# Kernel tuning notes

Measured on AMD Instinct MI355X. Metric: run time of the kernel, lower is better.

Reference implementation:

```python
import jax, jax.numpy as jnp
import numpy as np

B, N, K, D, H, FF, L, NH = 8, 50, 20, 3, 128, 2048, 3, 8
S = N * K
HD = H // NH


def setup_inputs() -> dict:
    key = jax.random.key(0)
    ks = jax.random.split(key, 16)
    visited = jax.random.uniform(ks[0], (B, S)) < 0.05
    # the single most-recent action per batch row (status flips 0 -> 1)
    action_idx = jax.random.randint(ks[1], (B,), 0, S)
    visited = visited.at[jnp.arange(B), action_idx].set(True)
    feats = jax.random.normal(ks[2], (B, S, D - 1)) * visited[:, :, None]
    state = jnp.concatenate([feats, visited[:, :, None].astype(jnp.float32)], axis=-1)
    prev_state = state.at[jnp.arange(B), action_idx, :].set(0.0)

    def w(k, shape, s=0.02):
        return jax.random.normal(k, shape, dtype=jnp.float32) * s

    return dict(
        prev_state=prev_state, state=state,
        W_pre=w(ks[3], (D, H)), b_pre=jnp.zeros(H),
        Wq=w(ks[4], (L, H, H)), bq=jnp.zeros((L, H)),
        Wk=w(ks[5], (L, H, H)), bk=jnp.zeros((L, H)),
        Wv=w(ks[6], (L, H, H)), bv=jnp.zeros((L, H)),
        Wo=w(ks[7], (L, H, H)), bo=jnp.zeros((L, H)),
        ln1_g=jnp.ones((L, H)), ln1_b=jnp.zeros((L, H)),
        Wff1=w(ks[8], (L, H, FF)), bff1=jnp.zeros((L, FF)),
        Wff2=w(ks[9], (L, FF, H)), bff2=jnp.zeros((L, H)),
        ln2_g=jnp.ones((L, H)), ln2_b=jnp.zeros((L, H)),
        W_comb=w(ks[10], (2 * H, H)), b_comb=jnp.zeros(H),
        W_dec=w(ks[11], (H, H)), b_dec=jnp.zeros(H),
        W_lin=w(ks[12], (S, S)), b_lin=jnp.zeros(S),
    )


def _layer_norm(x, g, b, eps=1e-5):
    m = jnp.mean(x, -1, keepdims=True)
    v = jnp.mean(jnp.square(x - m), -1, keepdims=True)
    return (x - m) * jax.lax.rsqrt(v + eps) * g + b


def _update_mask(state):
    # vectorized equivalent of the original Python-loop scatter mask
    status = state[:, :, -1] != 0                      # visited [B, S], S = K*N channel-major
    mask = status
    vis_kn = status.reshape(B, K, N)
    user_any = vis_kn.any(axis=1)                      # [B, N]: user visited on any channel
    mask = mask | jnp.broadcast_to(user_any[:, None, :], (B, K, N)).reshape(B, S)
    assigned = state.reshape(B, K, N, D).sum(-1) != 0  # [B, K, N]
    full = assigned.sum(-1) >= 2                       # [B, K]: channel already has 2 users
    mask = mask | jnp.broadcast_to(full[:, :, None], (B, K, N)).reshape(B, S)
    return mask


def reference(prev_state, state, W_pre, b_pre, Wq, bq, Wk, bk, Wv, bv, Wo, bo,
              ln1_g, ln1_b, Wff1, bff1, Wff2, bff2, ln2_g, ln2_b,
              W_comb, b_comb, W_dec, b_dec, W_lin, b_lin):
    mask = _update_mask(state)
    # exactly one status change per batch row (sequential RL step)
    diff = prev_state[:, :, -1] != state[:, :, -1]
    act_idx = jnp.argmax(diff, axis=1)                 # [B]

    x = state @ W_pre + b_pre                          # [B, S, H]
    scale = np.float32(1.0 / np.sqrt(HD))
    for i in range(L):  # 3 post-LN transformer encoder layers
        q = (x @ Wq[i] + bq[i]).reshape(B, S, NH, HD)
        k = (x @ Wk[i] + bk[i]).reshape(B, S, NH, HD)
        v = (x @ Wv[i] + bv[i]).reshape(B, S, NH, HD)
        att = jax.nn.softmax(jnp.einsum('bqhd,bkhd->bhqk', q, k) * scale, axis=-1)
        o = jnp.einsum('bhqk,bkhd->bqhd', att, v).reshape(B, S, H) @ Wo[i] + bo[i]
        x = _layer_norm(x + o, ln1_g[i], ln1_b[i])
        ff = jax.nn.relu(x @ Wff1[i] + bff1[i]) @ Wff2[i] + bff2[i]
        x = _layer_norm(x + ff, ln2_g[i], ln2_b[i])

    last = x[jnp.arange(B), act_idx]                   # [B, H]
    combined = jnp.concatenate([x.mean(axis=1), last], axis=-1)  # [B, 2H]
    g = combined @ W_comb + b_comb                     # [B, H]
    dec = x @ W_dec + b_dec                            # [B, S, H]
    scores = jnp.einsum('bsh,bh->bs', dec, g)          # [B, S]
    masked = scores @ W_lin + b_lin                    # Q-Learning head
    return jnp.where(mask, -jnp.inf, masked)
```

## Files before the change

### kernel.cpp

```cpp
#include <hip/hip_runtime.h>
#include <math.h>

#define Bb 8
#define Ss 1000
#define Kk 20
#define Nn 50
#define Dd 3
#define Hh 128
#define FFf 2048
#define Ll 3
#define NHh 8
#define HDd 16
#define ROWS (Bb*Ss)

#define SENTINEL -3.0e38f

typedef unsigned short ush;
typedef short short8 __attribute__((ext_vector_type(8)));
typedef float f32x4 __attribute__((ext_vector_type(4)));

__device__ __forceinline__ ush f2b(float f) {
  unsigned x = __float_as_uint(f);
  return (ush)((x + 0x7fff + ((x >> 16) & 1)) >> 16);
}

__global__ __launch_bounds__(256) void mask_kernel(const float* __restrict__ state,
                                                   const float* __restrict__ prev_state,
                                                   int* __restrict__ mask, int* __restrict__ act_idx) {
  int b = blockIdx.x, tid = threadIdx.x;
  __shared__ unsigned char status[Ss], assigned[Ss], uany[Nn], fullk[Kk];
  __shared__ int act;
  if (tid == 0) act = 1 << 30;
  __syncthreads();
  for (int s = tid; s < Ss; s += 256) {
    const float* st = state + ((size_t)b * Ss + s) * Dd;
    float f2 = st[2];
    status[s] = (f2 != 0.f);
    assigned[s] = ((st[0] + st[1] + f2) != 0.f);
    float p2 = prev_state[((size_t)b * Ss + s) * Dd + 2];
    if (p2 != f2) atomicMin(&act, s);
  }
  __syncthreads();
  if (tid < Nn) {
    unsigned char a = 0;
    for (int k = 0; k < Kk; ++k) a |= status[k * Nn + tid];
    uany[tid] = a;
  } else if (tid >= 64 && tid < 64 + Kk) {
    int k = tid - 64, cnt = 0;
    for (int n = 0; n < Nn; ++n) cnt += assigned[k * Nn + n];
    fullk[k] = (cnt >= 2);
  }
  __syncthreads();
  for (int s = tid; s < Ss; s += 256)
    mask[b * Ss + s] = (int)(status[s] | uany[s % Nn] | fullk[s / Nn]);
  if (tid == 0) act_idx[b] = (act >= Ss) ? 0 : act;
}

__global__ __launch_bounds__(256) void pre_kernel(const float* __restrict__ state,
                                                  const float* __restrict__ W_pre,
                                                  const float* __restrict__ b_pre,
                                                  float* __restrict__ x, ush* __restrict__ xbf) {
  int idx = blockIdx.x * 256 + threadIdx.x;
  if (idx >= ROWS * Hh) return;
  int row = idx >> 7, n = idx & 127;
  const float* st = state + (size_t)row * Dd;
  float v = b_pre[n] + st[0] * W_pre[n] + st[1] * W_pre[Hh + n] + st[2] * W_pre[2 * Hh + n];
  x[idx] = v;
  xbf[idx] = f2b(v);
}

#define S1 (384*128)
#define S2 (128*128)
#define S3 (2048*128)
#define S4 (128*2048)
#define SPL (S1+S2+S3+S4)
__global__ __launch_bounds__(256) void wprep_kernel(const float* __restrict__ Wq, const float* __restrict__ Wk,
                                                    const float* __restrict__ Wv, const float* __restrict__ Wo,
                                                    const float* __restrict__ Wff1, const float* __restrict__ Wff2,
                                                    const float* __restrict__ bq, const float* __restrict__ bk,
                                                    const float* __restrict__ bv,
                                                    ush* __restrict__ wqkvT, ush* __restrict__ woT,
                                                    ush* __restrict__ wff1T, ush* __restrict__ wff2T,
                                                    float* __restrict__ bqkv) {
  int idx = blockIdx.x * 256 + threadIdx.x;
  if (idx < Ll * SPL) {
    int l = idx / SPL, r = idx % SPL;
    if (r < S1) {
      int k = r / 384, n = r % 384;
      float v = (n < 128) ? Wq[((size_t)l * Hh + k) * Hh + n]
              : (n < 256) ? Wk[((size_t)l * Hh + k) * Hh + (n - 128)]
                          : Wv[((size_t)l * Hh + k) * Hh + (n - 256)];
      wqkvT[((size_t)l * 384 + n) * 128 + k] = f2b(v);
    } else if (r < S1 + S2) {
      int rr = r - S1; int k = rr >> 7, n = rr & 127;
      woT[((size_t)l * 128 + n) * 128 + k] = f2b(Wo[((size_t)l * Hh + k) * Hh + n]);
    } else if (r < S1 + S2 + S3) {
      int rr = r - S1 - S2; int k = rr >> 11, n = rr & 2047;
      wff1T[((size_t)l * 2048 + n) * 128 + k] = f2b(Wff1[((size_t)l * Hh + k) * FFf + n]);
    } else {
      int rr = r - S1 - S2 - S3; int k = rr >> 7, n = rr & 127;
      wff2T[((size_t)l * 128 + n) * 2048 + k] = f2b(Wff2[((size_t)l * FFf + k) * Hh + n]);
    }
  }
  if (idx < Ll * 384) {
    int l = idx / 384, c = idx % 384;
    bqkv[idx] = (c < 128) ? bq[l * Hh + c] : (c < 256 ? bk[l * Hh + c - 128] : bv[l * Hh + c - 256]);
  }
}

#define LDP 40
template <int ABF16, int OBF16, int RELU, int PARTIAL, int QKVV>
__global__ __launch_bounds__(256) void gemm_mfma(const void* __restrict__ A, const ush* __restrict__ Wt,
                                                 const float* __restrict__ bias, void* __restrict__ out,
                                                 int M, int N, int K, int klen, ush* __restrict__ vTout) {
  __shared__ ush As[64 * LDP];
  __shared__ ush Bs[64 * LDP];
  int tid = threadIdx.x;
  int lane = tid & 63, wid = tid >> 6;
  int wr = wid >> 1, wc = wid & 1;
  int m0 = blockIdx.y * 64, n0 = blockIdx.x * 64;
  int lrow = tid >> 2, lk = (tid & 3) << 3;
  int quad = lane >> 4, l16 = lane & 15, kb = quad << 3;
  int kstart = PARTIAL ? blockIdx.z * klen : 0;

  f32x4 acc[2][2];
#pragma unroll
  for (int i = 0; i < 2; ++i)
#pragma unroll
    for (int j = 0; j < 2; ++j) acc[i][j] = (f32x4){0.f, 0.f, 0.f, 0.f};

  for (int k0 = kstart; k0 < kstart + klen; k0 += 32) {
    if (ABF16) {
      short8 av = *(const short8*)((const ush*)A + (size_t)(m0 + lrow) * K + k0 + lk);
      *(short8*)&As[lrow * LDP + lk] = av;
    } else {
      const float* ap = (const float*)A + (size_t)(m0 + lrow) * K + k0 + lk;
      short8 s;
#pragma unroll
      for (int i = 0; i < 8; ++i) s[i] = (short)f2b(ap[i]);
      *(short8*)&As[lrow * LDP + lk] = s;
    }
    short8 bv = *(const short8*)&Wt[(size_t)(n0 + lrow) * K + k0 + lk];
    *(short8*)&Bs[lrow * LDP + lk] = bv;
    __syncthreads();

    short8 a0 = *(short8*)&As[(wr * 32 + l16) * LDP + kb];
    short8 a1 = *(short8*)&As[(wr * 32 + 16 + l16) * LDP + kb];
    short8 b0 = *(short8*)&Bs[(wc * 32 + l16) * LDP + kb];
    short8 b1 = *(short8*)&Bs[(wc * 32 + 16 + l16) * LDP + kb];
    acc[0][0] = __builtin_amdgcn_mfma_f32_16x16x32_bf16(a0, b0, acc[0][0], 0, 0, 0);
    acc[0][1] = __builtin_amdgcn_mfma_f32_16x16x32_bf16(a0, b1, acc[0][1], 0, 0, 0);
    acc[1][0] = __builtin_amdgcn_mfma_f32_16x16x32_bf16(a1, b0, acc[1][0], 0, 0, 0);
    acc[1][1] = __builtin_amdgcn_mfma_f32_16x16x32_bf16(a1, b1, acc[1][1], 0, 0, 0);
    __syncthreads();
  }

  float* pout = PARTIAL ? ((float*)out + (size_t)blockIdx.z * M * N) : (float*)out;
#pragma unroll
  for (int i = 0; i < 2; ++i)
#pragma unroll
    for (int j = 0; j < 2; ++j) {
      int col = n0 + wc * 32 + j * 16 + l16;
      int rbase = m0 + wr * 32 + i * 16 + quad * 4;
      float bval = (!PARTIAL || blockIdx.z == 0) ? bias[col] : 0.f;
#pragma unroll
      for (int v = 0; v < 4; ++v) {
        float o = acc[i][j][v] + bval;
        if (RELU) o = fmaxf(o, 0.f);
        if (QKVV && col >= 256) {
          int row = rbase + v;
          int bb2 = row / 1000, qq = row - bb2 * 1000;
          vTout[((size_t)(bb2 * 128 + (col - 256))) * 1024 + qq] = f2b(o);
        } else if (OBF16) {
          ((ush*)out)[(size_t)(rbase + v) * N + col] = f2b(o);
        } else {
          pout[(size_t)(rbase + v) * N + col] = o;
        }
      }
    }
}

#define WLP 132
__global__ __launch_bounds__(256) void wo_ln_kernel(const ush* __restrict__ A, const ush* __restrict__ Wt,
                                                    const float* __restrict__ bias,
                                                    const float* __restrict__ ln_g, const float* __restrict__ ln_b,
                                                    float* __restrict__ x, ush* __restrict__ xbf) {
  __shared__ char smem[64 * WLP * 4];
  ush* As = (ush*)smem;
  ush* Bs = As + 64 * LDP;
  float* xs = (float*)smem;
  __shared__ float pbias[128], pg[128], pb2[128];

  int tid = threadIdx.x, lane = tid & 63, w = tid >> 6;
  int l16 = lane & 15, quad = lane >> 4, kb = quad * 8;
  int m0 = blockIdx.x * 64;
  if (tid < 128) { pbias[tid] = bias[tid]; pg[tid] = ln_g[tid]; pb2[tid] = ln_b[tid]; }

  f32x4 acc[8];
#pragma unroll
  for (int j = 0; j < 8; ++j) acc[j] = (f32x4){0.f, 0.f, 0.f, 0.f};

  int srow = tid >> 2, slk = (tid & 3) << 3;
  for (int k0 = 0; k0 < 128; k0 += 32) {
    *(short8*)&As[srow * LDP + slk] = *(const short8*)(A + (size_t)(m0 + srow) * 128 + k0 + slk);
#pragma unroll
    for (int rr = 0; rr < 2; ++rr) {
      int row = rr * 64 + srow;
      *(short8*)&Bs[row * LDP + slk] = *(const short8*)(Wt + (size_t)row * 128 + k0 + slk);
    }
    __syncthreads();
    short8 aA = *(short8*)&As[(w * 16 + l16) * LDP + kb];
#pragma unroll
    for (int j = 0; j < 8; ++j) {
      short8 bj = *(short8*)&Bs[(j * 16 + l16) * LDP + kb];
      acc[j] = __builtin_amdgcn_mfma_f32_16x16x32_bf16(aA, bj, acc[j], 0, 0, 0);
    }
    __syncthreads();
  }

  for (int e = tid; e < 64 * 32; e += 256) {
    int idx = e * 4; int row = idx >> 7, col = idx & 127;
    *(float4*)&xs[row * WLP + col] = *(const float4*)&x[(size_t)(m0 + row) * 128 + col];
  }
  __syncthreads();

  float v[8][4], s1[4] = {0.f, 0.f, 0.f, 0.f}, s2[4] = {0.f, 0.f, 0.f, 0.f};
#pragma unroll
  for (int j = 0; j < 8; ++j) {
    int col = j * 16 + l16;
#pragma unroll
    for (int r = 0; r < 4; ++r) {
      int rowt = w * 16 + quad * 4 + r;
      float vv = acc[j][r] + pbias[col] + xs[rowt * WLP + col];
      v[j][r] = vv; s1[r] += vv; s2[r] += vv * vv;
    }
  }
#pragma unroll
  for (int m = 1; m <= 8; m <<= 1) {
#pragma unroll
    for (int r = 0; r < 4; ++r) { s1[r] += __shfl_xor(s1[r], m); s2[r] += __shfl_xor(s2[r], m); }
  }
#pragma unroll
  for (int r = 0; r < 4; ++r) {
    int rowt = w * 16 + quad * 4 + r;
    float mean = s1[r] * (1.f / 128.f);
    float var = s2[r] * (1.f / 128.f) - mean * mean;
    float rstd = rsqrtf(var + 1e-5f);
#pragma unroll
    for (int j = 0; j < 8; ++j) {
      int col = j * 16 + l16;
      float o = (v[j][r] - mean) * rstd * pg[col] + pb2[col];
      size_t gi = (size_t)(m0 + rowt) * 128 + col;
      x[gi] = o; xbf[gi] = f2b(o);
    }
  }
}

__global__ __launch_bounds__(256) void attn_mfma(const ush* __restrict__ qkv,
                                                 const ush* __restrict__ vT,
                                                 ush* __restrict__ attn_o) {
  int blk = blockIdx.x;
  int local = blk >> 3;
  int bh = ((blk & 7) << 3) | (local >> 4);
  int qt = local & 15;
  int b = bh >> 3, h = bh & 7;
  int qbase = qt * 64;
  int tid = threadIdx.x, lane = tid & 63, w = tid >> 6;
  int l16 = lane & 15, quad = lane >> 4, kb = quad * 8;

  __shared__ ush Ks[64][40];
  __shared__ ush Vs[16][72];
  __shared__ ush Pb[4][16][72];

  if (tid < 128)
    *(short8*)&Ks[tid >> 1][16 + (tid & 1) * 8] = (short8){0, 0, 0, 0, 0, 0, 0, 0};

  int qrow = qbase + w * 16 + l16; if (qrow >= Ss) qrow = Ss - 1;
  short8 aq = *(const short8*)(qkv + (size_t)(b * Ss + qrow) * 384 + h * HDd + kb);

  const short one_b = (short)0x3F80;
  const short8 ones = (short8){one_b, one_b, one_b, one_b, one_b, one_b, one_b, one_b};
  f32x4 acc_pv = (f32x4){0.f, 0.f, 0.f, 0.f};
  f32x4 acc_l = (f32x4){0.f, 0.f, 0.f, 0.f};
  const f32x4 zero4 = (f32x4){0.f, 0.f, 0.f, 0.f};

  for (int k0 = 0; k0 < Ss; k0 += 64) {
    __syncthreads();
    if (tid < 128) {
      int row = tid >> 1, g = tid & 1;
      int key = k0 + row;
      short8 s8 = (short8){0, 0, 0, 0, 0, 0, 0, 0};
      if (key < Ss)
        s8 = *(const short8*)(qkv + (size_t)(b * Ss + key) * 384 + 128 + h * HDd + g * 8);
      *(short8*)&Ks[row][g * 8] = s8;
    } else {
      int t = tid - 128;
      int d = t >> 3, kg = t & 7;
      short8 v8 = *(const short8*)(vT + (size_t)(b * 128 + h * 16 + d) * 1024 + k0 + kg * 8);
      *(short8*)&Vs[d][kg * 8] = v8;
    }
    __syncthreads();

#pragma unroll
    for (int kn = 0; kn < 4; ++kn) {
      short8 bk = *(short8*)&Ks[kn * 16 + l16][kb];
      f32x4 s = __builtin_amdgcn_mfma_f32_16x16x32_bf16(aq, bk, zero4, 0, 0, 0);
      int key = k0 + kn * 16 + l16;
      float m = (key < Ss) ? 1.f : 0.f;
#pragma unroll
      for (int r = 0; r < 4; ++r)
        Pb[w][quad * 4 + r][kn * 16 + l16] = f2b(__expf(s[r] * 0.25f) * m);
    }
    short8 pa0 = *(short8*)&Pb[w][l16][kb];
    short8 pa1 = *(short8*)&Pb[w][l16][32 + kb];
    short8 vb0 = *(short8*)&Vs[l16][kb];
    short8 vb1 = *(short8*)&Vs[l16][32 + kb];
    acc_pv = __builtin_amdgcn_mfma_f32_16x16x32_bf16(pa0, vb0, acc_pv, 0, 0, 0);
    acc_pv = __builtin_amdgcn_mfma_f32_16x16x32_bf16(pa1, vb1, acc_pv, 0, 0, 0);
    acc_l = __builtin_amdgcn_mfma_f32_16x16x32_bf16(pa0, ones, acc_l, 0, 0, 0);
    acc_l = __builtin_amdgcn_mfma_f32_16x16x32_bf16(pa1, ones, acc_l, 0, 0, 0);
  }

#pragma unroll
  for (int r = 0; r < 4; ++r) {
    int q = qbase + w * 16 + quad * 4 + r;
    if (q < Ss)
      attn_o[((size_t)(b * Ss + q)) * Hh + h * HDd + l16] = f2b(acc_pv[r] / acc_l[r]);
  }
}

__global__ __launch_bounds__(256) void resid_ln_kernel(float* __restrict__ x, ush* __restrict__ xbf,
                                                       const float* __restrict__ r, int nparts, size_t pstride,
                                                       const float* __restrict__ g, const float* __restrict__ bb) {
  int half = threadIdx.x >> 7;
  int row = blockIdx.x * 2 + half;
  int n = threadIdx.x & 127;
  int wid = threadIdx.x >> 6;
  float v = x[(size_t)row * Hh + n];
  for (int p = 0; p < nparts; ++p) v += r[p * pstride + (size_t)row * Hh + n];
  float s = v;
  for (int off = 32; off; off >>= 1) s += __shfl_down(s, off);
  __shared__ float red[4], red2[4];
  if ((threadIdx.x & 63) == 0) red[wid] = s;
  __syncthreads();
  float mean = (red[half * 2] + red[half * 2 + 1]) * (1.f / Hh);
  float d = v - mean;
  float s2 = d * d;
  for (int off = 32; off; off >>= 1) s2 += __shfl_down(s2, off);
  if ((threadIdx.x & 63) == 0) red2[wid] = s2;
  __syncthreads();
  float var = (red2[half * 2] + red2[half * 2 + 1]) * (1.f / Hh);
  float o = d * rsqrtf(var + 1e-5f) * g[n] + bb[n];
  x[(size_t)row * Hh + n] = o;
  xbf[(size_t)row * Hh + n] = f2b(o);
}

__global__ __launch_bounds__(128) void mean_part_kernel(const float* __restrict__ x,
                                                        float* __restrict__ mpart) {
  int c = blockIdx.x, b = blockIdx.y, n = threadIdx.x;
  const float* xb = x + ((size_t)b * Ss + c * 125) * Hh + n;
  float s = 0.f;
#pragma unroll 5
  for (int i = 0; i < 125; ++i) s += xb[(size_t)i * Hh];
  mpart[(c * Bb + b) * Hh + n] = s;
}

__global__ __launch_bounds__(128) void ghc_kernel(const float* __restrict__ x, const float* __restrict__ mpart,
                                                  const int* __restrict__ act_idx,
                                                  const float* __restrict__ W_comb, const float* __restrict__ b_comb,
                                                  const float* __restrict__ W_dec, const float* __restrict__ b_dec,
                                                  float* __restrict__ h, float* __restrict__ cb) {
  int b = blockIdx.x, n = threadIdx.x;
  __shared__ float cs[2 * Hh], gs[Hh], red[2];
  float mean = 0.f;
#pragma unroll
  for (int c = 0; c < 8; ++c) mean += mpart[(c * Bb + b) * Hh + n];
  cs[n] = mean * (1.f / Ss);
  cs[Hh + n] = x[((size_t)b * Ss + act_idx[b]) * Hh + n];
  __syncthreads();
  float acc = b_comb[n];
  for (int j = 0; j < 2 * Hh; ++j) acc += cs[j] * W_comb[(size_t)j * Hh + n];
  gs[n] = acc;
  __syncthreads();
  float hv = 0.f;
  for (int c = 0; c < Hh; ++c) hv += W_dec[(size_t)n * Hh + c] * gs[c];
  h[b * Hh + n] = hv;
  float t = b_dec[n] * gs[n];
  for (int off = 32; off; off >>= 1) t += __shfl_down(t, off);
  if ((n & 63) == 0) red[n >> 6] = t;
  __syncthreads();
  if (n == 0) cb[b] = red[0] + red[1];
}

__global__ __launch_bounds__(256) void scores_kernel(const float* __restrict__ x, const float* __restrict__ h,
                                                     const float* __restrict__ cb, float* __restrict__ scores) {
  int wid = threadIdx.x >> 6, lane = threadIdx.x & 63;
  int row = blockIdx.x * 4 + wid;
  if (row >= ROWS) return;
  int b = row / Ss;
  const float* xr = x + (size_t)row * Hh;
  const float* hb = h + b * Hh;
  float s = xr[lane] * hb[lane] + xr[lane + 64] * hb[lane + 64];
  for (int off = 32; off; off >>= 1) s += __shfl_down(s, off);
  if (lane == 0) scores[row] = s + cb[b];
}

__global__ __launch_bounds__(256) void final_part(const float* __restrict__ scores,
                                                  const float* __restrict__ W_lin,
                                                  float* __restrict__ fpart) {
  int spc = blockIdx.x, kc = blockIdx.y, b = blockIdx.z;
  int tid = threadIdx.x;
  __shared__ float ss[125];
  for (int i = tid; i < 125; i += 256) ss[i] = scores[b * Ss + kc * 125 + i];
  __syncthreads();
  if (tid < 250) {
    int sp = spc * 250 + tid;
    float acc = 0.f;
    const float* wl = &W_lin[(size_t)(kc * 125) * Ss + sp];
#pragma unroll 5
    for (int s = 0; s < 125; ++s) acc = fmaf(ss[s], wl[(size_t)s * Ss], acc);
    fpart[((size_t)kc * Bb + b) * Ss + sp] = acc;
  }
}

__global__ __launch_bounds__(256) void final_combine(const float* __restrict__ fpart,
                                                     const float* __restrict__ b_lin,
                                                     const int* __restrict__ mask,
                                                     float* __restrict__ out) {
  int b = blockIdx.y;
  int sp = blockIdx.x * 256 + threadIdx.x;
  if (sp >= Ss) return;
  float acc = b_lin[sp];
#pragma unroll
  for (int kc = 0; kc < 8; ++kc) acc += fpart[((size_t)kc * Bb + b) * Ss + sp];
  out[b * Ss + sp] = mask[b * Ss + sp] ? SENTINEL : acc;
}

extern "C" void kernel_launch(void* const* d_in, const int* in_sizes, int n_in,
                              void* d_out, int out_size, void* d_ws, size_t ws_size,
                              hipStream_t stream) {
  const float* prev_state = (const float*)d_in[0];
  const float* state = (const float*)d_in[1];
  const float* W_pre = (const float*)d_in[2];
  const float* b_pre = (const float*)d_in[3];
  const float* Wq = (const float*)d_in[4];
  const float* bq = (const float*)d_in[5];
  const float* Wk = (const float*)d_in[6];
  const float* bk = (const float*)d_in[7];
  const float* Wv = (const float*)d_in[8];
  const float* bv = (const float*)d_in[9];
  const float* Wo = (const float*)d_in[10];
  const float* bo = (const float*)d_in[11];
  const float* ln1_g = (const float*)d_in[12];
  const float* ln1_b = (const float*)d_in[13];
  const float* Wff1 = (const float*)d_in[14];
  const float* bff1 = (const float*)d_in[15];
  const float* Wff2 = (const float*)d_in[16];
  const float* bff2 = (const float*)d_in[17];
  const float* ln2_g = (const float*)d_in[18];
  const float* ln2_b = (const float*)d_in[19];
  const float* W_comb = (const float*)d_in[20];
  const float* b_comb = (const float*)d_in[21];
  const float* W_dec = (const float*)d_in[22];
  const float* b_dec = (const float*)d_in[23];
  const float* W_lin = (const float*)d_in[24];
  const float* b_lin = (const float*)d_in[25];

  char* wsp = (char*)d_ws;
  auto alloc = [&](size_t bytes) { char* p = wsp; wsp += (bytes + 255) & ~(size_t)255; return p; };
  int* mask = (int*)alloc(ROWS * 4);
  int* act = (int*)alloc(Bb * 4);
  ush* wqkvT = (ush*)alloc((size_t)Ll * 384 * 128 * 2);
  ush* woT = (ush*)alloc((size_t)Ll * 128 * 128 * 2);
  ush* wff1T = (ush*)alloc((size_t)Ll * 2048 * 128 * 2);
  ush* wff2T = (ush*)alloc((size_t)Ll * 128 * 2048 * 2);
  float* bqkv = (float*)alloc((size_t)Ll * 384 * 4);
  float* x = (float*)alloc((size_t)ROWS * Hh * 4);
  ush* xbf = (ush*)alloc((size_t)ROWS * Hh * 2);
  ush* qkv_bf = (ush*)alloc((size_t)ROWS * 384 * 2);
  ush* vT = (ush*)alloc((size_t)Bb * 128 * 1024 * 2);
  ush* attn_ob = (ush*)alloc((size_t)ROWS * Hh * 2);
  float* ff2p = (float*)alloc((size_t)4 * ROWS * Hh * 4);
  float* mpart = (float*)alloc((size_t)8 * Bb * Hh * 4);
  float* hbuf = (float*)alloc((size_t)Bb * Hh * 4);
  float* cb = (float*)alloc((size_t)Bb * 4);
  float* scores = (float*)alloc((size_t)ROWS * 4);
  float* fpart = (float*)alloc((size_t)8 * Bb * Ss * 4);
  ush* ffb = (ush*)alloc((size_t)ROWS * FFf * 2);

  wprep_kernel<<<dim3((Ll * SPL + 255) / 256), 256, 0, stream>>>(Wq, Wk, Wv, Wo, Wff1, Wff2, bq, bk, bv,
                                                                 wqkvT, woT, wff1T, wff2T, bqkv);
  mask_kernel<<<Bb, 256, 0, stream>>>(state, prev_state, mask, act);
  pre_kernel<<<dim3((ROWS * Hh + 255) / 256), 256, 0, stream>>>(state, W_pre, b_pre, x, xbf);

  for (int l = 0; l < Ll; ++l) {
    gemm_mfma<1, 1, 0, 0, 1><<<dim3(384 / 64, ROWS / 64), 256, 0, stream>>>(
        xbf, wqkvT + (size_t)l * 384 * 128, bqkv + l * 384, qkv_bf, ROWS, 384, 128, 128, vT);
    attn_mfma<<<dim3(1024), 256, 0, stream>>>(qkv_bf, vT, attn_ob);
    wo_ln_kernel<<<dim3(ROWS / 64), 256, 0, stream>>>(
        attn_ob, woT + (size_t)l * 128 * 128, bo + l * Hh, ln1_g + l * Hh, ln1_b + l * Hh, x, xbf);
    gemm_mfma<1, 1, 1, 0, 0><<<dim3(2048 / 64, ROWS / 64), 256, 0, stream>>>(
        xbf, wff1T + (size_t)l * 2048 * 128, bff1 + l * FFf, ffb, ROWS, 2048, 128, 128, nullptr);
    gemm_mfma<1, 0, 0, 1, 0><<<dim3(128 / 64, ROWS / 64, 4), 256, 0, stream>>>(
        ffb, wff2T + (size_t)l * 128 * 2048, bff2 + l * Hh, ff2p, ROWS, 128, 2048, 512, nullptr);
    resid_ln_kernel<<<ROWS / 2, 256, 0, stream>>>(x, xbf, ff2p, 4, (size_t)ROWS * Hh, ln2_g + l * Hh, ln2_b + l * Hh);
  }

  mean_part_kernel<<<dim3(8, Bb), 128, 0, stream>>>(x, mpart);
  ghc_kernel<<<Bb, 128, 0, stream>>>(x, mpart, act, W_comb, b_comb, W_dec, b_dec, hbuf, cb);
  scores_kernel<<<dim3(ROWS / 4), 256, 0, stream>>>(x, hbuf, cb, scores);
  final_part<<<dim3(4, 8, Bb), 256, 0, stream>>>(scores, W_lin, fpart);
  final_combine<<<dim3(4, Bb), 256, 0, stream>>>(fpart, b_lin, mask, (float*)d_out);
}
```

Measured before the change: 399.9 us.

## Split attention key range across two blocks and combine partials in a separate kernel

```diff
diff --git a/kernel.cpp b/kernel.cpp
--- a/kernel.cpp
+++ b/kernel.cpp
@@ -258,11 +258,13 @@
 
 __global__ __launch_bounds__(256) void attn_mfma(const ush* __restrict__ qkv,
                                                  const ush* __restrict__ vT,
-                                                 ush* __restrict__ attn_o) {
+                                                 float* __restrict__ pv_part,
+                                                 float* __restrict__ l_part) {
   int blk = blockIdx.x;
   int local = blk >> 3;
-  int bh = ((blk & 7) << 3) | (local >> 4);
-  int qt = local & 15;
+  int bh = ((blk & 7) << 3) | (local >> 5);
+  int rest = local & 31;
+  int qt = rest >> 1, kc = rest & 1;
   int b = bh >> 3, h = bh & 7;
   int qbase = qt * 64;
   int tid = threadIdx.x, lane = tid & 63, w = tid >> 6;
@@ -284,7 +286,9 @@
   f32x4 acc_l = (f32x4){0.f, 0.f, 0.f, 0.f};
   const f32x4 zero4 = (f32x4){0.f, 0.f, 0.f, 0.f};
 
-  for (int k0 = 0; k0 < Ss; k0 += 64) {
+  int kstart = kc * 512;
+  for (int k0 = kstart; k0 < kstart + 512 && k0 < Ss; k0 += 64) {
+    bool full = (k0 + 64 <= Ss);
     __syncthreads();
     if (tid < 128) {
       int row = tid >> 1, g = tid & 1;
@@ -305,11 +309,17 @@
     for (int kn = 0; kn < 4; ++kn) {
       short8 bk = *(short8*)&Ks[kn * 16 + l16][kb];
       f32x4 s = __builtin_amdgcn_mfma_f32_16x16x32_bf16(aq, bk, zero4, 0, 0, 0);
-      int key = k0 + kn * 16 + l16;
-      float m = (key < Ss) ? 1.f : 0.f;
-#pragma unroll
-      for (int r = 0; r < 4; ++r)
-        Pb[w][quad * 4 + r][kn * 16 + l16] = f2b(__expf(s[r] * 0.25f) * m);
+      if (full) {
+#pragma unroll
+        for (int r = 0; r < 4; ++r)
+          Pb[w][quad * 4 + r][kn * 16 + l16] = f2b(__expf(s[r] * 0.25f));
+      } else {
+        int key = k0 + kn * 16 + l16;
+        float m = (key < Ss) ? 1.f : 0.f;
+#pragma unroll
+        for (int r = 0; r < 4; ++r)
+          Pb[w][quad * 4 + r][kn * 16 + l16] = f2b(__expf(s[r] * 0.25f) * m);
+      }
     }
     short8 pa0 = *(short8*)&Pb[w][l16][kb];
     short8 pa1 = *(short8*)&Pb[w][l16][32 + kb];
@@ -324,9 +334,24 @@
 #pragma unroll
   for (int r = 0; r < 4; ++r) {
     int q = qbase + w * 16 + quad * 4 + r;
-    if (q < Ss)
-      attn_o[((size_t)(b * Ss + q)) * Hh + h * HDd + l16] = f2b(acc_pv[r] / acc_l[r]);
-  }
+    if (q < Ss) {
+      pv_part[(size_t)kc * ROWS * Hh + ((size_t)(b * Ss + q)) * Hh + h * HDd + l16] = acc_pv[r];
+      if (l16 == 0) l_part[(size_t)(kc * 64 + bh) * 1024 + q] = acc_l[r];
+    }
+  }
+}
+
+__global__ __launch_bounds__(256) void attn_combine(const float* __restrict__ pv,
+                                                    const float* __restrict__ lp,
+                                                    ush* __restrict__ attn_o) {
+  int idx = blockIdx.x * 256 + threadIdx.x;
+  if (idx >= ROWS * Hh) return;
+  int row = idx >> 7, col = idx & 127;
+  int b = row / Ss, q = row - b * Ss, h = col >> 4;
+  int li = (b * 8 + h) * 1024 + q;
+  float l = lp[li] + lp[64 * 1024 + li];
+  float o = pv[idx] + pv[(size_t)ROWS * Hh + idx];
+  attn_o[idx] = f2b(o / l);
 }
 
 __global__ __launch_bounds__(256) void resid_ln_kernel(float* __restrict__ x, ush* __restrict__ xbf,
@@ -480,6 +505,8 @@
   ush* qkv_bf = (ush*)alloc((size_t)ROWS * 384 * 2);
   ush* vT = (ush*)alloc((size_t)Bb * 128 * 1024 * 2);
   ush* attn_ob = (ush*)alloc((size_t)ROWS * Hh * 2);
+  float* pv_part = (float*)alloc((size_t)2 * ROWS * Hh * 4);
+  float* l_part = (float*)alloc((size_t)2 * 64 * 1024 * 4);
   float* ff2p = (float*)alloc((size_t)4 * ROWS * Hh * 4);
   float* mpart = (float*)alloc((size_t)8 * Bb * Hh * 4);
   float* hbuf = (float*)alloc((size_t)Bb * Hh * 4);
@@ -496,7 +523,8 @@
   for (int l = 0; l < Ll; ++l) {
     gemm_mfma<1, 1, 0, 0, 1><<<dim3(384 / 64, ROWS / 64), 256, 0, stream>>>(
         xbf, wqkvT + (size_t)l * 384 * 128, bqkv + l * 384, qkv_bf, ROWS, 384, 128, 128, vT);
-    attn_mfma<<<dim3(1024), 256, 0, stream>>>(qkv_bf, vT, attn_ob);
+    attn_mfma<<<dim3(2048), 256, 0, stream>>>(qkv_bf, vT, pv_part, l_part);
+    attn_combine<<<dim3((ROWS * Hh + 255) / 256), 256, 0, stream>>>(pv_part, l_part, attn_ob);
     wo_ln_kernel<<<dim3(ROWS / 64), 256, 0, stream>>>(
         attn_ob, woT + (size_t)l * 128 * 128, bo + l * Hh, ln1_g + l * Hh, ln1_b + l * Hh, x, xbf);
     gemm_mfma<1, 1, 1, 0, 0><<<dim3(2048 / 64, ROWS / 64), 256, 0, stream>>>(
```

Result: no change. 400.3 us (+0.1%).
